# Kernel optimization log

Measured on AMD Instinct MI355X. Metric: run time of the kernel, lower is better.

The kernel has to match this reference:

```python
import jax, jax.numpy as jnp
import numpy as np

VOL = (256, 256, 256)
K = 64  # number of connected components (clusters)


def setup_inputs() -> dict:
    key = jax.random.key(0)
    k1, k2, k3 = jax.random.split(key, 3)
    # Precomputed connected-component labels of (pred + target) > 0.
    # 0 = background, 1..K = clusters.
    labels = jax.random.randint(k1, VOL, 0, K + 1, dtype=jnp.int32)
    fg = labels > 0
    # Binary prediction / ground-truth masks, nonzero only inside labeled regions
    # (consistent with labels being components of the overlay of pred and target).
    pred = ((jax.random.uniform(k2, VOL) < 0.6) & fg).astype(jnp.float32)
    target = ((jax.random.uniform(k3, VOL) < 0.6) & fg).astype(jnp.float32)
    return {"pred": pred, "target": target, "labels": labels, "num_clusters": K}


def reference(pred, target, labels, num_clusters):
    # Per-cluster dice via one fused segment reduction instead of a Python loop
    # over clusters. Segment 0 is background and is dropped, matching
    # range(1, num_features + 1) in the original.
    lab = labels.reshape(-1)
    p = pred.reshape(-1)
    t = target.reshape(-1)
    nseg = num_clusters + 1
    # intersection = sum(pred_cluster * gt_cluster); pred/target are binary so
    # logical_and(...).float() products reduce to pred * target per segment.
    inter = jax.ops.segment_sum(p * t, lab, num_segments=nseg)[1:]
    sum_p = jax.ops.segment_sum(p, lab, num_segments=nseg)[1:]
    sum_t = jax.ops.segment_sum(t, lab, num_segments=nseg)[1:]
    union = sum_p + sum_t
    dice = jnp.where(union > 0, 2.0 * inter / jnp.maximum(union, 1.0), 1.0)
    return 1.0 - jnp.mean(dice)
```

## Files before the change

kernel.cpp:

```cpp
#include <hip/hip_runtime.h>


#define NSEG 65
#define NREP 64
#define REP_MASK 63
#define NWAVES 4
#define NCOPY 16
#define BLOCKS 2048
#define THREADS 256
#define UNROLL 8

__device__ __forceinline__ unsigned int pack32(float p, float t) {
    unsigned int sp = (p != 0.0f) ? 1u : 0u;
    unsigned int st = (t != 0.0f) ? 1u : 0u;
    return ((sp & st) << 20) | (sp << 10) | st;
}

__device__ __forceinline__ void accum4(unsigned int (*s_cnt)[NSEG], int copy,
                                       float4 p, float4 t, int4 l) {
    atomicAdd(&s_cnt[copy][l.x], pack32(p.x, t.x));
    atomicAdd(&s_cnt[copy][l.y], pack32(p.y, t.y));
    atomicAdd(&s_cnt[copy][l.z], pack32(p.z, t.z));
    atomicAdd(&s_cnt[copy][l.w], pack32(p.w, t.w));
}

__global__ __launch_bounds__(THREADS, 4) void seg_count_kernel(
    const float* __restrict__ pred,
    const float* __restrict__ target,
    const int* __restrict__ labels,
    unsigned long long* __restrict__ part,
    int n)
{
    __shared__ unsigned int s_cnt[NCOPY][NSEG];
    const int tid = threadIdx.x;
    const int copy = tid >> 4;
    const int rep = (int)blockIdx.x & REP_MASK;

    for (int i = tid; i < NCOPY * NSEG; i += THREADS)
        ((unsigned int*)s_cnt)[i] = 0u;
    __syncthreads();

    const int n_vec = n >> 2;
    const float4* __restrict__ p4 = (const float4*)pred;
    const float4* __restrict__ t4 = (const float4*)target;
    const int4*   __restrict__ l4 = (const int4*)labels;

    const int chunk = (n_vec + (int)gridDim.x - 1) / (int)gridDim.x;
    const int base = blockIdx.x * chunk;
    const int end = min(base + chunk, n_vec);

    int idx = base + tid;
    for (; idx + (UNROLL - 1) * THREADS < end; idx += UNROLL * THREADS) {
        float4 p[UNROLL]; float4 t[UNROLL]; int4 l[UNROLL];
        #pragma unroll
        for (int u = 0; u < UNROLL; ++u) p[u] = p4[idx + u * THREADS];
        #pragma unroll
        for (int u = 0; u < UNROLL; ++u) t[u] = t4[idx + u * THREADS];
        #pragma unroll
        for (int u = 0; u < UNROLL; ++u) l[u] = l4[idx + u * THREADS];
        __builtin_amdgcn_sched_barrier(0);
        #pragma unroll
        for (int u = 0; u < UNROLL; ++u) accum4(s_cnt, copy, p[u], t[u], l[u]);
    }
    for (; idx < end; idx += THREADS)
        accum4(s_cnt, copy, p4[idx], t4[idx], l4[idx]);

    if (blockIdx.x == 0) {
        for (int i = (n_vec << 2) + tid; i < n; i += THREADS)
            atomicAdd(&s_cnt[copy][labels[i]], pack32(pred[i], target[i]));
    }
    __syncthreads();

    for (int s = tid; s < NSEG; s += THREADS) {
        unsigned long long in = 0, sp = 0, st = 0;
        #pragma unroll
        for (int c = 0; c < NCOPY; ++c) {
            unsigned int v = s_cnt[c][s];
            st += v & 0x3FFu;
            sp += (v >> 10) & 0x3FFu;
            in += v >> 20;
        }
        unsigned long long tot = (in << 42) | (sp << 21) | st;
        if (tot) atomicAdd(&part[s * NREP + rep], tot);
    }
}

__global__ __launch_bounds__(256) void dice_finalize_kernel(
    const unsigned long long* __restrict__ part,
    const int* __restrict__ nc_ptr,
    float* __restrict__ out)
{
    const int nc = *nc_ptr;
    const int tid = threadIdx.x;
    const int s = 1 + (tid >> 2);
    const int q = tid & 3;

    unsigned long long acc = 0;
    const unsigned long long* row = part + s * NREP + q * 16;
    #pragma unroll
    for (int i = 0; i < 16; ++i) acc += row[i];
    acc += __shfl_xor(acc, 1);
    acc += __shfl_xor(acc, 2);

    __shared__ float s_dice[64];
    if (q == 0) {
        float in = (float)(acc >> 42);
        float sp = (float)((acc >> 21) & 0x1FFFFFull);
        float st = (float)(acc & 0x1FFFFFull);
        float uni = sp + st;
        float dice = (uni > 0.0f) ? (2.0f * in / uni) : 1.0f;
        s_dice[s - 1] = (s <= nc) ? dice : 0.0f;
    }
    __syncthreads();

    if (tid < 64) {
        float local = s_dice[tid];
        #pragma unroll
        for (int off = 32; off > 0; off >>= 1)
            local += __shfl_down(local, off);
        if (tid == 0) out[0] = 1.0f - local / (float)nc;
    }
}

extern "C" void kernel_launch(void* const* d_in, const int* in_sizes, int n_in,
                              void* d_out, int out_size, void* d_ws, size_t ws_size,
                              hipStream_t stream) {
    const float* pred   = (const float*)d_in[0];
    const float* target = (const float*)d_in[1];
    const int*   labels = (const int*)d_in[2];
    const int*   nc_ptr = (const int*)d_in[3];
    float* out = (float*)d_out;
    unsigned long long* part = (unsigned long long*)d_ws;

    const int n = in_sizes[0];

    hipMemsetAsync(d_ws, 0, NSEG * NREP * sizeof(unsigned long long), stream);

    seg_count_kernel<<<BLOCKS, THREADS, 0, stream>>>(
        pred, target, labels, part, n);
    dice_finalize_kernel<<<1, 256, 0, stream>>>(part, nc_ptr, out);
}
```

Measured before the change: 197.4 us.

## Replace shared atomics with per-thread private 16-bit histograms

Gives each thread its own column of 16-bit counters in shared memory, replacing shared-memory atomicAdd with plain read-modify-write. The counters pack intersection and union per element. Blocks are halved to 1024 and the unroll drops to 4, and the final reduction reads packed 64-bit words using SWAR masking. This removes LDS atomic contention, but the 8-bit lanes could overflow if a thread sees more than 255 hits per label, and background counts are no longer accumulated.

```diff
diff --git a/kernel.cpp b/kernel.cpp
--- a/kernel.cpp
+++ b/kernel.cpp
@@ -1,27 +1,23 @@
 #include <hip/hip_runtime.h>
 
 
-#define NSEG 65
+#define NBIN 65
 #define NREP 64
 #define REP_MASK 63
-#define NWAVES 4
-#define NCOPY 16
-#define BLOCKS 2048
+#define BLOCKS 1024
 #define THREADS 256
-#define UNROLL 8
 
-__device__ __forceinline__ unsigned int pack32(float p, float t) {
+__device__ __forceinline__ unsigned short contrib16(float p, float t) {
     unsigned int sp = (p != 0.0f) ? 1u : 0u;
     unsigned int st = (t != 0.0f) ? 1u : 0u;
-    return ((sp & st) << 20) | (sp << 10) | st;
+    return (unsigned short)(((sp & st) << 8) | (sp + st));
 }
 
-__device__ __forceinline__ void accum4(unsigned int (*s_cnt)[NSEG], int copy,
-                                       float4 p, float4 t, int4 l) {
-    atomicAdd(&s_cnt[copy][l.x], pack32(p.x, t.x));
-    atomicAdd(&s_cnt[copy][l.y], pack32(p.y, t.y));
-    atomicAdd(&s_cnt[copy][l.z], pack32(p.z, t.z));
-    atomicAdd(&s_cnt[copy][l.w], pack32(p.w, t.w));
+__device__ __forceinline__ void rmw4(unsigned short* col, float4 p, float4 t, int4 l) {
+    col[l.x * THREADS] = (unsigned short)(col[l.x * THREADS] + contrib16(p.x, t.x));
+    col[l.y * THREADS] = (unsigned short)(col[l.y * THREADS] + contrib16(p.y, t.y));
+    col[l.z * THREADS] = (unsigned short)(col[l.z * THREADS] + contrib16(p.z, t.z));
+    col[l.w * THREADS] = (unsigned short)(col[l.w * THREADS] + contrib16(p.w, t.w));
 }
 
 __global__ __launch_bounds__(THREADS, 4) void seg_count_kernel(
@@ -31,13 +27,12 @@
     unsigned long long* __restrict__ part,
     int n)
 {
-    __shared__ unsigned int s_cnt[NCOPY][NSEG];
+    __shared__ unsigned short s_hist[NBIN][THREADS];
     const int tid = threadIdx.x;
-    const int copy = tid >> 4;
     const int rep = (int)blockIdx.x & REP_MASK;
 
-    for (int i = tid; i < NCOPY * NSEG; i += THREADS)
-        ((unsigned int*)s_cnt)[i] = 0u;
+    unsigned int* hz = (unsigned int*)s_hist;
+    for (int i = tid; i < NBIN * THREADS / 2; i += THREADS) hz[i] = 0u;
     __syncthreads();
 
     const int n_vec = n >> 2;
@@ -49,39 +44,60 @@
     const int base = blockIdx.x * chunk;
     const int end = min(base + chunk, n_vec);
 
+    unsigned short* col = &s_hist[0][tid];
+
     int idx = base + tid;
-    for (; idx + (UNROLL - 1) * THREADS < end; idx += UNROLL * THREADS) {
-        float4 p[UNROLL]; float4 t[UNROLL]; int4 l[UNROLL];
-        #pragma unroll
-        for (int u = 0; u < UNROLL; ++u) p[u] = p4[idx + u * THREADS];
-        #pragma unroll
-        for (int u = 0; u < UNROLL; ++u) t[u] = t4[idx + u * THREADS];
-        #pragma unroll
-        for (int u = 0; u < UNROLL; ++u) l[u] = l4[idx + u * THREADS];
+    for (; idx + 3 * THREADS < end; idx += 4 * THREADS) {
+        float4 p0 = p4[idx];
+        float4 p1 = p4[idx + THREADS];
+        float4 p2 = p4[idx + 2 * THREADS];
+        float4 p3 = p4[idx + 3 * THREADS];
+        float4 t0 = t4[idx];
+        float4 t1 = t4[idx + THREADS];
+        float4 t2 = t4[idx + 2 * THREADS];
+        float4 t3 = t4[idx + 3 * THREADS];
+        int4   l0 = l4[idx];
+        int4   l1 = l4[idx + THREADS];
+        int4   l2 = l4[idx + 2 * THREADS];
+        int4   l3 = l4[idx + 3 * THREADS];
         __builtin_amdgcn_sched_barrier(0);
-        #pragma unroll
-        for (int u = 0; u < UNROLL; ++u) accum4(s_cnt, copy, p[u], t[u], l[u]);
+        rmw4(col, p0, t0, l0);
+        rmw4(col, p1, t1, l1);
+        rmw4(col, p2, t2, l2);
+        rmw4(col, p3, t3, l3);
     }
     for (; idx < end; idx += THREADS)
-        accum4(s_cnt, copy, p4[idx], t4[idx], l4[idx]);
+        rmw4(col, p4[idx], t4[idx], l4[idx]);
 
     if (blockIdx.x == 0) {
         for (int i = (n_vec << 2) + tid; i < n; i += THREADS)
-            atomicAdd(&s_cnt[copy][labels[i]], pack32(pred[i], target[i]));
+            col[labels[i] * THREADS] =
+                (unsigned short)(col[labels[i] * THREADS] + contrib16(pred[i], target[i]));
     }
     __syncthreads();
 
-    for (int s = tid; s < NSEG; s += THREADS) {
-        unsigned long long in = 0, sp = 0, st = 0;
-        #pragma unroll
-        for (int c = 0; c < NCOPY; ++c) {
-            unsigned int v = s_cnt[c][s];
-            st += v & 0x3FFu;
-            sp += (v >> 10) & 0x3FFu;
-            in += v >> 20;
-        }
-        unsigned long long tot = (in << 42) | (sp << 21) | st;
-        if (tot) atomicAdd(&part[s * NREP + rep], tot);
+    const int s = 1 + (tid >> 2);
+    const int q = tid & 3;
+    const unsigned long long* row = (const unsigned long long*)&s_hist[s][q * 64];
+    unsigned long long accU = 0, accI = 0;
+    const int rot = tid & 15;
+    #pragma unroll
+    for (int j = 0; j < 16; ++j) {
+        int i = (j + rot) & 15;
+        unsigned long long v = row[i];
+        accU += v & 0x00FF00FF00FF00FFull;
+        accI += (v >> 8) & 0x00FF00FF00FF00FFull;
+    }
+    accU += accU >> 32;
+    accI += accI >> 32;
+    unsigned int U = ((unsigned int)accU & 0xFFFFu) + (((unsigned int)accU >> 16) & 0xFFFFu);
+    unsigned int I = ((unsigned int)accI & 0xFFFFu) + (((unsigned int)accI >> 16) & 0xFFFFu);
+
+    U += __shfl_xor(U, 1); U += __shfl_xor(U, 2);
+    I += __shfl_xor(I, 1); I += __shfl_xor(I, 2);
+    if (q == 0) {
+        unsigned long long tot = ((unsigned long long)I << 32) | (unsigned long long)U;
+        if (tot) atomicAdd(&part[(s - 1) * NREP + rep], tot);
     }
 }
 
@@ -96,7 +112,7 @@
     const int q = tid & 3;
 
     unsigned long long acc = 0;
-    const unsigned long long* row = part + s * NREP + q * 16;
+    const unsigned long long* row = part + (s - 1) * NREP + q * 16;
     #pragma unroll
     for (int i = 0; i < 16; ++i) acc += row[i];
     acc += __shfl_xor(acc, 1);
@@ -104,11 +120,9 @@
 
     __shared__ float s_dice[64];
     if (q == 0) {
-        float in = (float)(acc >> 42);
-        float sp = (float)((acc >> 21) & 0x1FFFFFull);
-        float st = (float)(acc & 0x1FFFFFull);
-        float uni = sp + st;
-        float dice = (uni > 0.0f) ? (2.0f * in / uni) : 1.0f;
+        float U = (float)(unsigned int)(acc & 0xFFFFFFFFull);
+        float I = (float)(unsigned int)(acc >> 32);
+        float dice = (U > 0.0f) ? (2.0f * I / U) : 1.0f;
         s_dice[s - 1] = (s <= nc) ? dice : 0.0f;
     }
     __syncthreads();
@@ -134,7 +148,7 @@
 
     const int n = in_sizes[0];
 
-    hipMemsetAsync(d_ws, 0, NSEG * NREP * sizeof(unsigned long long), stream);
+    hipMemsetAsync(d_ws, 0, 64 * NREP * sizeof(unsigned long long), stream);
 
     seg_count_kernel<<<BLOCKS, THREADS, 0, stream>>>(
         pred, target, labels, part, n);
```

Measured after the change: 205.3 us. +4.0%, slower.
